# Optimization experiments

Hardware: AMD Instinct MI355X
Metric: run time of the kernel (lower is better)

## Reference

```python
import jax, jax.numpy as jnp
import numpy as np

NUM_EMBEDDINGS = 8192
EMBEDDING_DIM = 256
PROJECTION_DIM = 128


def setup_inputs() -> dict:
    key = jax.random.key(0)
    k_x, k_cb, k_w, k_b = jax.random.split(key, 4)
    x = jax.random.normal(k_x, (16, 1024, EMBEDDING_DIM), dtype=jnp.float32)
    codebook = jax.random.normal(k_cb, (NUM_EMBEDDINGS, EMBEDDING_DIM), dtype=jnp.float32)
    proj_w = jax.random.normal(k_w, (EMBEDDING_DIM, PROJECTION_DIM), dtype=jnp.float32) / np.sqrt(EMBEDDING_DIM)
    proj_b = jax.random.normal(k_b, (PROJECTION_DIM,), dtype=jnp.float32) * 0.01
    return {"x": x, "codebook": codebook, "proj_w": proj_w, "proj_b": proj_b}


def reference(x, codebook, proj_w, proj_b):
    # Flatten tokens: [N, D]
    x_flat = x.reshape(-1, EMBEDDING_DIM)
    # Project tokens and codebook into the distance space: [N, P], [K, P]
    x_proj = x_flat @ proj_w + proj_b
    cb_proj = codebook @ proj_w + proj_b
    # Squared euclidean distances via expansion: [N, K]
    distances = (
        jnp.sum(x_proj ** 2, axis=1, keepdims=True)
        - 2.0 * (x_proj @ cb_proj.T)
        + jnp.sum(cb_proj ** 2, axis=1)
    )
    idx = jnp.argmin(distances, axis=1)
    discrete = jax.nn.one_hot(idx, NUM_EMBEDDINGS, dtype=x.dtype)  # [N, K]
    # One-hot matmul lookup (disguised gather): [N, D]
    quantized = (discrete @ codebook).reshape(x.shape)
    return (discrete, quantized)
```

## Files before the change

### kernel.cpp

```cpp
#include <hip/hip_runtime.h>
#include <math.h>

#define D 256
#define P 128
#define K 8192
#define NTOK 16384
#define NROWS (NTOK + K)
#define CAPC 64
#define MARGIN 3.0f
#define FLT_BIG 3.402823466e+38f

typedef __attribute__((ext_vector_type(8))) short bf16x8;
typedef __attribute__((ext_vector_type(4))) float f32x4;
typedef __attribute__((ext_vector_type(8))) unsigned short u16x8;

__device__ __forceinline__ unsigned short f32_to_bf16_rne(float f) {
    unsigned int u = __float_as_uint(f);
    u = (u + 0x7fffu + ((u >> 16) & 1u)) >> 16;
    return (unsigned short)u;
}

__global__ __launch_bounds__(256) void proj_kernel(
    const float* __restrict__ x, const float* __restrict__ cb,
    const float* __restrict__ w, const float* __restrict__ bias,
    float* __restrict__ xproj, float* __restrict__ cproj,
    float* __restrict__ xnorm, float* __restrict__ cnorm,
    unsigned short* __restrict__ xh, unsigned short* __restrict__ chs,
    int* __restrict__ cnt)
{
    __shared__ float As[16][D];
    const int tid = threadIdx.x;
    const int row0 = blockIdx.x * 16;

    {
        int g = blockIdx.x * 256 + tid;
        if (g < NTOK) cnt[g] = 0;
    }

    for (int i = tid; i < 16 * (D / 4); i += 256) {
        int r = i / (D / 4);
        int c4 = i % (D / 4);
        int gr = row0 + r;
        const float* src = (gr < NTOK) ? (x + (size_t)gr * D)
                                       : (cb + (size_t)(gr - NTOK) * D);
        float4 v = ((const float4*)src)[c4];
        ((float4*)&As[r][0])[c4] = v;
    }
    __syncthreads();

    const int r = tid >> 4;
    const int c0 = (tid & 15) * 8;

    float acc[8];
#pragma unroll
    for (int j = 0; j < 8; j++) acc[j] = 0.f;

    for (int d = 0; d < D; d += 4) {
        float4 a4 = *(const float4*)&As[r][d];
#pragma unroll
        for (int dd = 0; dd < 4; dd++) {
            float av = (dd == 0) ? a4.x : (dd == 1) ? a4.y : (dd == 2) ? a4.z : a4.w;
            float4 w0 = *(const float4*)&w[(size_t)(d + dd) * P + c0];
            float4 w1 = *(const float4*)&w[(size_t)(d + dd) * P + c0 + 4];
            acc[0] = fmaf(av, w0.x, acc[0]);
            acc[1] = fmaf(av, w0.y, acc[1]);
            acc[2] = fmaf(av, w0.z, acc[2]);
            acc[3] = fmaf(av, w0.w, acc[3]);
            acc[4] = fmaf(av, w1.x, acc[4]);
            acc[5] = fmaf(av, w1.y, acc[5]);
            acc[6] = fmaf(av, w1.z, acc[6]);
            acc[7] = fmaf(av, w1.w, acc[7]);
        }
    }

    float out[8];
    float nrm = 0.f;
    u16x8 hv;
#pragma unroll
    for (int j = 0; j < 8; j++) {
        out[j] = acc[j] + bias[c0 + j];
        nrm = fmaf(out[j], out[j], nrm);
        hv[j] = f32_to_bf16_rne(out[j]);
    }

    const int gr = row0 + r;
    float4 o0; o0.x = out[0]; o0.y = out[1]; o0.z = out[2]; o0.w = out[3];
    float4 o1; o1.x = out[4]; o1.y = out[5]; o1.z = out[6]; o1.w = out[7];
    if (gr < NTOK) {
        float* dst = xproj + (size_t)gr * P;
        *(float4*)&dst[c0] = o0;
        *(float4*)&dst[c0 + 4] = o1;
        *(u16x8*)(xh + (size_t)gr * P + c0) = hv;
    } else {
        int row = gr - NTOK;
        float* dst = cproj + (size_t)row * P;
        *(float4*)&dst[c0] = o0;
        *(float4*)&dst[c0 + 4] = o1;
        int t64 = row >> 6, rg = (row >> 4) & 3, rl = row & 15;
        int ks = c0 >> 5, q = (c0 >> 3) & 3;
        size_t atom = ((size_t)(t64 * 16 + rg * 4 + ks) * 4 + q) * 16 + rl;
        *(u16x8*)(chs + atom * 8) = hv;
    }

#pragma unroll
    for (int off = 1; off < 16; off <<= 1)
        nrm += __shfl_xor(nrm, off, 16);
    if ((tid & 15) == 0) {
        if (gr < NTOK) xnorm[gr] = nrm;
        else           cnorm[gr - NTOK] = nrm;
    }
}

__global__ __launch_bounds__(256, 3) void minzero_collect_kernel(
    const unsigned short* __restrict__ xh, const unsigned short* __restrict__ chs,
    const float* __restrict__ xnorm, const float* __restrict__ cnorm,
    int* __restrict__ cnt, int* __restrict__ cand, float* __restrict__ discrete)
{
    const int tid = threadIdx.x;
    const int tok0 = blockIdx.x * 128;
    const int kbase = blockIdx.y * 2048;
    const int flat = blockIdx.y * gridDim.x + blockIdx.x;

    const int wave = tid >> 6;
    const int lane = tid & 63;
    const int quad = lane >> 4;
    const int l15 = lane & 15;
    const int trow = tok0 + wave * 32;

    f32x4* zbase = (f32x4*)discrete + (size_t)flat * 65536;
    const f32x4 zv = (f32x4)(0.f);

    bf16x8 afrag[2][4];
#pragma unroll
    for (int mi = 0; mi < 2; mi++)
#pragma unroll
        for (int ks = 0; ks < 4; ks++)
            afrag[mi][ks] = *(const bf16x8*)(
                xh + (size_t)(trow + mi * 16 + l15) * P + ks * 32 + quad * 8);

    float xnv[2][4];
#pragma unroll
    for (int mi = 0; mi < 2; mi++)
#pragma unroll
        for (int r = 0; r < 4; r++)
            xnv[mi][r] = xnorm[trow + mi * 16 + quad * 4 + r];

    float rmin[2][4];
#pragma unroll
    for (int mi = 0; mi < 2; mi++)
#pragma unroll
        for (int r = 0; r < 4; r++) rmin[mi][r] = FLT_BIG;

    for (int ct = 0; ct < 32; ct++) {
        const int kt = kbase + ct * 64;
        const int t64 = kt >> 6;

#pragma unroll
        for (int s = 0; s < 8; s++)
            zbase[(size_t)ct * 2048 + s * 256 + tid] = zv;

        f32x4 acc[2][4];
#pragma unroll
        for (int mi = 0; mi < 2; mi++)
#pragma unroll
            for (int nj = 0; nj < 4; nj++) acc[mi][nj] = (f32x4)(0.f);

#pragma unroll
        for (int ks = 0; ks < 4; ks++) {
            const bf16x8* base = (const bf16x8*)(chs) + (size_t)(t64 * 16 + ks) * 64 + lane;
            bf16x8 b0 = base[0 * 4 * 64];
            bf16x8 b1 = base[1 * 4 * 64];
            bf16x8 b2 = base[2 * 4 * 64];
            bf16x8 b3 = base[3 * 4 * 64];
            acc[0][0] = __builtin_amdgcn_mfma_f32_16x16x32_bf16(afrag[0][ks], b0, acc[0][0], 0, 0, 0);
            acc[0][1] = __builtin_amdgcn_mfma_f32_16x16x32_bf16(afrag[0][ks], b1, acc[0][1], 0, 0, 0);
            acc[0][2] = __builtin_amdgcn_mfma_f32_16x16x32_bf16(afrag[0][ks], b2, acc[0][2], 0, 0, 0);
            acc[0][3] = __builtin_amdgcn_mfma_f32_16x16x32_bf16(afrag[0][ks], b3, acc[0][3], 0, 0, 0);
            acc[1][0] = __builtin_amdgcn_mfma_f32_16x16x32_bf16(afrag[1][ks], b0, acc[1][0], 0, 0, 0);
            acc[1][1] = __builtin_amdgcn_mfma_f32_16x16x32_bf16(afrag[1][ks], b1, acc[1][1], 0, 0, 0);
            acc[1][2] = __builtin_amdgcn_mfma_f32_16x16x32_bf16(afrag[1][ks], b2, acc[1][2], 0, 0, 0);
            acc[1][3] = __builtin_amdgcn_mfma_f32_16x16x32_bf16(afrag[1][ks], b3, acc[1][3], 0, 0, 0);
        }

        float cn[4];
#pragma unroll
        for (int nj = 0; nj < 4; nj++) cn[nj] = cnorm[kt + nj * 16 + l15];

        if (ct == 0) {
#pragma unroll
            for (int mi = 0; mi < 2; mi++)
#pragma unroll
                for (int r = 0; r < 4; r++) {
                    float rm = rmin[mi][r];
#pragma unroll
                    for (int nj = 0; nj < 4; nj++) {
                        float dd = (xnv[mi][r] - 2.0f * acc[mi][nj][r]) + cn[nj];
                        rm = fminf(rm, dd);
                    }
#pragma unroll
                    for (int off = 1; off < 16; off <<= 1)
                        rm = fminf(rm, __shfl_xor(rm, off));
                    rmin[mi][r] = rm;
                    const float thr = rm + MARGIN;
                    const int tok = trow + mi * 16 + quad * 4 + r;
#pragma unroll
                    for (int nj = 0; nj < 4; nj++) {
                        float dd = (xnv[mi][r] - 2.0f * acc[mi][nj][r]) + cn[nj];
                        if (dd <= thr) {
                            int pos = atomicAdd(&cnt[tok], 1);
                            if (pos < CAPC) cand[(size_t)tok * CAPC + pos] = kt + nj * 16 + l15;
                        }
                    }
                }
        } else {
#pragma unroll
            for (int mi = 0; mi < 2; mi++)
#pragma unroll
                for (int r = 0; r < 4; r++) {
                    float rm = rmin[mi][r];
                    const float thr = rm + MARGIN;
                    const int tok = trow + mi * 16 + quad * 4 + r;
#pragma unroll
                    for (int nj = 0; nj < 4; nj++) {
                        float dd = (xnv[mi][r] - 2.0f * acc[mi][nj][r]) + cn[nj];
                        rm = fminf(rm, dd);
                        if (dd <= thr) {
                            int pos = atomicAdd(&cnt[tok], 1);
                            if (pos < CAPC) cand[(size_t)tok * CAPC + pos] = kt + nj * 16 + l15;
                        }
                    }
                    rmin[mi][r] = rm;
                }
            if (ct & 1) {
#pragma unroll
                for (int mi = 0; mi < 2; mi++)
#pragma unroll
                    for (int r = 0; r < 4; r++) {
                        float m = rmin[mi][r];
#pragma unroll
                        for (int off = 1; off < 16; off <<= 1)
                            m = fminf(m, __shfl_xor(m, off));
                        rmin[mi][r] = m;
                    }
            }
        }
    }
}

__global__ __launch_bounds__(256) void rescorefinal_kernel(
    const float* __restrict__ xproj, const float* __restrict__ cproj,
    const float* __restrict__ xnorm, const float* __restrict__ cnorm,
    const int* __restrict__ cnt, const int* __restrict__ cand,
    const float* __restrict__ cb,
    float* __restrict__ discrete, float* __restrict__ quant)
{
    __shared__ int sidx[64];
    const int tid = threadIdx.x;
    const int lane = tid & 63;
    const int wave = tid >> 6;
    const int tok0 = blockIdx.x * 64;

    for (int i = 0; i < 16; i++) {
        const int t = tok0 + wave * 16 + i;
        const int n = cnt[t];
        const bool full = (n > CAPC);
        const int lim = full ? K : n;
        const float xn = xnorm[t];
        const float* xr = xproj + (size_t)t * P;

        unsigned long long pack = 0xFFFFFFFFFFFFFFFFull;
        for (int j = lane; j < lim; j += 64) {
            const int k = full ? j : cand[(size_t)t * CAPC + j];
            const float* cr = cproj + (size_t)k * P;
            float s = 0.f;
#pragma unroll 8
            for (int p = 0; p < P; p += 4) {
                float4 a = *(const float4*)&xr[p];
                float4 b = *(const float4*)&cr[p];
                s = fmaf(a.x, b.x, s);
                s = fmaf(a.y, b.y, s);
                s = fmaf(a.z, b.z, s);
                s = fmaf(a.w, b.w, s);
            }
            float dist = (xn - 2.0f * s) + cnorm[k];
            unsigned long long pk =
                ((unsigned long long)__float_as_uint(dist) << 32) |
                (unsigned long long)(unsigned)k;
            if (pk < pack) pack = pk;
        }
#pragma unroll
        for (int off = 1; off < 64; off <<= 1) {
            unsigned long long o = __shfl_xor((long long)pack, off);
            if (o < pack) pack = o;
        }
        if (lane == 0) {
            int bi = (int)(pack & 0xFFFFFFFFull);
            if (bi >= 0 && bi < K) {
                sidx[wave * 16 + i] = bi;
                discrete[(size_t)t * K + bi] = 1.0f;
            } else sidx[wave * 16 + i] = 0;
        }
    }
    __syncthreads();

    for (int i = tid; i < 64 * (D / 4); i += 256) {
        int t = i >> 6;
        int c4 = i & 63;
        int bi = sidx[t];
        float4 v = ((const float4*)(cb + (size_t)bi * D))[c4];
        ((float4*)(quant + (size_t)(tok0 + t) * D))[c4] = v;
    }
}

extern "C" void kernel_launch(void* const* d_in, const int* in_sizes, int n_in,
                              void* d_out, int out_size, void* d_ws, size_t ws_size,
                              hipStream_t stream) {
    const float* x    = (const float*)d_in[0];
    const float* cb   = (const float*)d_in[1];
    const float* w    = (const float*)d_in[2];
    const float* bias = (const float*)d_in[3];

    float* out = (float*)d_out;
    float* discrete = out;
    float* quant = out + (size_t)NTOK * K;

    char* ws = (char*)d_ws;
    size_t off = 0;
    float* xproj = (float*)(ws + off); off += (size_t)NTOK * P * 4;
    float* cproj = (float*)(ws + off); off += (size_t)K * P * 4;
    float* xnorm = (float*)(ws + off); off += (size_t)NTOK * 4;
    float* cnorm = (float*)(ws + off); off += (size_t)K * 4;
    unsigned short* xh  = (unsigned short*)(ws + off); off += (size_t)NTOK * P * 2;
    unsigned short* chs = (unsigned short*)(ws + off); off += (size_t)K * P * 2;
    int* cnt  = (int*)(ws + off); off += (size_t)NTOK * 4;
    int* cand = (int*)(ws + off); off += (size_t)NTOK * CAPC * 4;

    proj_kernel<<<dim3(NROWS / 16), dim3(256), 0, stream>>>(
        x, cb, w, bias, xproj, cproj, xnorm, cnorm, xh, chs, cnt);

    minzero_collect_kernel<<<dim3(NTOK / 128, 4), dim3(256), 0, stream>>>(
        xh, chs, xnorm, cnorm, cnt, cand, discrete);

    rescorefinal_kernel<<<dim3(NTOK / 64), dim3(256), 0, stream>>>(
        xproj, cproj, xnorm, cnorm, cnt, cand, cb, discrete, quant);
}
```

Before: 844.2 us.

## Redistribute discrete zero-fill across all three kernels to balance store bandwidth

```diff
diff --git a/kernel.cpp b/kernel.cpp
--- a/kernel.cpp
+++ b/kernel.cpp
@@ -10,6 +10,7 @@
 #define MARGIN 3.0f
 #define FLT_BIG 3.402823466e+38f
 
+
 typedef __attribute__((ext_vector_type(8))) short bf16x8;
 typedef __attribute__((ext_vector_type(4))) float f32x4;
 typedef __attribute__((ext_vector_type(8))) unsigned short u16x8;
@@ -26,7 +27,7 @@
     float* __restrict__ xproj, float* __restrict__ cproj,
     float* __restrict__ xnorm, float* __restrict__ cnorm,
     unsigned short* __restrict__ xh, unsigned short* __restrict__ chs,
-    int* __restrict__ cnt)
+    int* __restrict__ cnt, float* __restrict__ discrete)
 {
     __shared__ float As[16][D];
     const int tid = threadIdx.x;
@@ -55,7 +56,19 @@
 #pragma unroll
     for (int j = 0; j < 8; j++) acc[j] = 0.f;
 
+    const f32x4 zv = (f32x4)(0.f);
+    f32x4* dis4 = (f32x4*)discrete;
+    const int frow0 = 5 * (int)blockIdx.x;
+
     for (int d = 0; d < D; d += 4) {
+        {
+            int j = d >> 2;
+            if (j < 25) {
+                int fr = frow0 + j / 5;
+                int fc4 = 768 + (j % 5) * 256 + tid;
+                dis4[(size_t)fr * 2048 + fc4] = zv;
+            }
+        }
         float4 a4 = *(const float4*)&As[r][d];
 #pragma unroll
         for (int dd = 0; dd < 4; dd++) {
@@ -127,7 +140,8 @@
     const int l15 = lane & 15;
     const int trow = tok0 + wave * 32;
 
-    f32x4* zbase = (f32x4*)discrete + (size_t)flat * 65536;
+    f32x4* dis4 = (f32x4*)discrete;
+    const int frow0 = 7680 + 17 * flat;
     const f32x4 zv = (f32x4)(0.f);
 
     bf16x8 afrag[2][4];
@@ -156,8 +170,14 @@
         const int t64 = kt >> 6;
 
 #pragma unroll
-        for (int s = 0; s < 8; s++)
-            zbase[(size_t)ct * 2048 + s * 256 + tid] = zv;
+        for (int s = 0; s < 3; s++) {
+            int u = ct * 3 + s;
+            if (u < 85) {
+                int fr = frow0 + u / 5;
+                int fc4 = 768 + (u % 5) * 256 + tid;
+                dis4[(size_t)fr * 2048 + fc4] = zv;
+            }
+        }
 
         f32x4 acc[2][4];
 #pragma unroll
@@ -260,7 +280,17 @@
     const int wave = tid >> 6;
     const int tok0 = blockIdx.x * 64;
 
+    f32x4* dis4 = (f32x4*)discrete;
+    const f32x4 zv = (f32x4)(0.f);
+
     for (int i = 0; i < 16; i++) {
+#pragma unroll
+        for (int s = 0; s < 12; s++) {
+            int fr = tok0 + i * 4 + s / 3;
+            int fc4 = (s % 3) * 256 + tid;
+            dis4[(size_t)fr * 2048 + fc4] = zv;
+        }
+
         const int t = tok0 + wave * 16 + i;
         const int n = cnt[t];
         const bool full = (n > CAPC);
@@ -295,18 +325,21 @@
         }
         if (lane == 0) {
             int bi = (int)(pack & 0xFFFFFFFFull);
-            if (bi >= 0 && bi < K) {
-                sidx[wave * 16 + i] = bi;
-                discrete[(size_t)t * K + bi] = 1.0f;
-            } else sidx[wave * 16 + i] = 0;
+            sidx[wave * 16 + i] = (bi >= 0 && bi < K) ? bi : -1;
         }
     }
     __syncthreads();
+
+    if (tid < 64) {
+        int bi = sidx[tid];
+        if (bi >= 0) discrete[(size_t)(tok0 + tid) * K + bi] = 1.0f;
+    }
 
     for (int i = tid; i < 64 * (D / 4); i += 256) {
         int t = i >> 6;
         int c4 = i & 63;
         int bi = sidx[t];
+        if (bi < 0) bi = 0;
         float4 v = ((const float4*)(cb + (size_t)bi * D))[c4];
         ((float4*)(quant + (size_t)(tok0 + t) * D))[c4] = v;
     }
@@ -336,7 +369,7 @@
     int* cand = (int*)(ws + off); off += (size_t)NTOK * CAPC * 4;
 
     proj_kernel<<<dim3(NROWS / 16), dim3(256), 0, stream>>>(
-        x, cb, w, bias, xproj, cproj, xnorm, cnorm, xh, chs, cnt);
+        x, cb, w, bias, xproj, cproj, xnorm, cnorm, xh, chs, cnt, discrete);
 
     minzero_collect_kernel<<<dim3(NTOK / 128, 4), dim3(256), 0, stream>>>(
         xh, chs, xnorm, cnorm, cnt, cand, discrete);
```

New measurement: 872.0 us. 1.03x slower.

## Split one-hot zero-fill of discrete output across all three kernels

Applied to the files above, without the earlier changes.

```diff
diff --git a/kernel.cpp b/kernel.cpp
--- a/kernel.cpp
+++ b/kernel.cpp
@@ -9,6 +9,8 @@
 #define CAPC 64
 #define MARGIN 3.0f
 #define FLT_BIG 3.402823466e+38f
+#define PFILL 256
+
 
 typedef __attribute__((ext_vector_type(8))) short bf16x8;
 typedef __attribute__((ext_vector_type(4))) float f32x4;
@@ -26,14 +28,28 @@
     float* __restrict__ xproj, float* __restrict__ cproj,
     float* __restrict__ xnorm, float* __restrict__ cnorm,
     unsigned short* __restrict__ xh, unsigned short* __restrict__ chs,
-    int* __restrict__ cnt)
+    int* __restrict__ cnt, float* __restrict__ discrete)
 {
     __shared__ float As[16][D];
     const int tid = threadIdx.x;
-    const int row0 = blockIdx.x * 16;
+
+    if (blockIdx.x < PFILL) {
+        const int f = blockIdx.x;
+        f32x4* dis4 = (f32x4*)discrete;
+        const f32x4 zv = (f32x4)(0.f);
+        for (int u = tid; u < 64 * 256; u += 256) {
+            int fr = (f << 6) + (u >> 8);
+            int fc4 = 512 + (u & 255);
+            dis4[(size_t)fr * 2048 + fc4] = zv;
+        }
+        return;
+    }
+
+    const int cblk = blockIdx.x - PFILL;
+    const int row0 = cblk * 16;
 
     {
-        int g = blockIdx.x * 256 + tid;
+        int g = cblk * 256 + tid;
         if (g < NTOK) cnt[g] = 0;
     }
 
@@ -127,7 +143,8 @@
     const int l15 = lane & 15;
     const int trow = tok0 + wave * 32;
 
-    f32x4* zbase = (f32x4*)discrete + (size_t)flat * 65536;
+    f32x4* dis4 = (f32x4*)discrete;
+    const int zrow = flat * 32;
     const f32x4 zv = (f32x4)(0.f);
 
     bf16x8 afrag[2][4];
@@ -154,10 +171,6 @@
     for (int ct = 0; ct < 32; ct++) {
         const int kt = kbase + ct * 64;
         const int t64 = kt >> 6;
-
-#pragma unroll
-        for (int s = 0; s < 8; s++)
-            zbase[(size_t)ct * 2048 + s * 256 + tid] = zv;
 
         f32x4 acc[2][4];
 #pragma unroll
@@ -244,6 +257,13 @@
                     }
             }
         }
+
+        {
+            f32x4* rowp = dis4 + (size_t)(zrow + ct) * 2048;
+#pragma unroll
+            for (int s = 0; s < 5; s++)
+                rowp[768 + s * 256 + tid] = zv;
+        }
     }
 }
 
@@ -259,6 +279,8 @@
     const int lane = tid & 63;
     const int wave = tid >> 6;
     const int tok0 = blockIdx.x * 64;
+
+    float4* dis4f = (float4*)discrete;
 
     for (int i = 0; i < 16; i++) {
         const int t = tok0 + wave * 16 + i;
@@ -293,13 +315,23 @@
             unsigned long long o = __shfl_xor((long long)pack, off);
             if (o < pack) pack = o;
         }
-        if (lane == 0) {
-            int bi = (int)(pack & 0xFFFFFFFFull);
-            if (bi >= 0 && bi < K) {
-                sidx[wave * 16 + i] = bi;
-                discrete[(size_t)t * K + bi] = 1.0f;
-            } else sidx[wave * 16 + i] = 0;
-        }
+        int bi = (int)(pack & 0xFFFFFFFFull);
+        const bool valid = (bi >= 0 && bi < K);
+        if (lane == 0) sidx[wave * 16 + i] = valid ? bi : 0;
+
+#pragma unroll
+        for (int s = 0; s < 8; s++) {
+            int fc4 = s * 64 + lane;
+            int b0 = fc4 << 2;
+            float4 v;
+            v.x = (bi == b0)     ? 1.f : 0.f;
+            v.y = (bi == b0 + 1) ? 1.f : 0.f;
+            v.z = (bi == b0 + 2) ? 1.f : 0.f;
+            v.w = (bi == b0 + 3) ? 1.f : 0.f;
+            dis4f[(size_t)t * 2048 + fc4] = v;
+        }
+        if (lane == 0 && valid && bi >= 2048)
+            discrete[(size_t)t * K + bi] = 1.0f;
     }
     __syncthreads();
 
@@ -335,8 +367,8 @@
     int* cnt  = (int*)(ws + off); off += (size_t)NTOK * 4;
     int* cand = (int*)(ws + off); off += (size_t)NTOK * CAPC * 4;
 
-    proj_kernel<<<dim3(NROWS / 16), dim3(256), 0, stream>>>(
-        x, cb, w, bias, xproj, cproj, xnorm, cnorm, xh, chs, cnt);
+    proj_kernel<<<dim3(NROWS / 16 + PFILL), dim3(256), 0, stream>>>(
+        x, cb, w, bias, xproj, cproj, xnorm, cnorm, xh, chs, cnt, discrete);
 
     minzero_collect_kernel<<<dim3(NTOK / 128, 4), dim3(256), 0, stream>>>(
         xh, chs, xnorm, cnorm, cnt, cand, discrete);
```

After: 850.0 us. Within noise of the previous version (+0.7%).

## Fuse rescore into collect kernel via last-block atomic counter; zero own rows

Applied to the files above, without the earlier changes.

```diff
diff --git a/kernel.cpp b/kernel.cpp
--- a/kernel.cpp
+++ b/kernel.cpp
@@ -26,7 +26,7 @@
     float* __restrict__ xproj, float* __restrict__ cproj,
     float* __restrict__ xnorm, float* __restrict__ cnorm,
     unsigned short* __restrict__ xh, unsigned short* __restrict__ chs,
-    int* __restrict__ cnt)
+    int* __restrict__ cnt, int* __restrict__ done)
 {
     __shared__ float As[16][D];
     const int tid = threadIdx.x;
@@ -35,6 +35,7 @@
     {
         int g = blockIdx.x * 256 + tid;
         if (g < NTOK) cnt[g] = 0;
+        if (g < NTOK / 128) done[g] = 0;
     }
 
     for (int i = tid; i < 16 * (D / 4); i += 256) {
@@ -111,15 +112,17 @@
     }
 }
 
-__global__ __launch_bounds__(256, 3) void minzero_collect_kernel(
+__global__ __launch_bounds__(256, 3) void mzc_rescore_kernel(
     const unsigned short* __restrict__ xh, const unsigned short* __restrict__ chs,
     const float* __restrict__ xnorm, const float* __restrict__ cnorm,
-    int* __restrict__ cnt, int* __restrict__ cand, float* __restrict__ discrete)
+    const float* __restrict__ xproj, const float* __restrict__ cproj,
+    const float* __restrict__ cb,
+    int* __restrict__ cnt, int* __restrict__ cand, int* __restrict__ done,
+    float* __restrict__ discrete, float* __restrict__ quant)
 {
     const int tid = threadIdx.x;
     const int tok0 = blockIdx.x * 128;
     const int kbase = blockIdx.y * 2048;
-    const int flat = blockIdx.y * gridDim.x + blockIdx.x;
 
     const int wave = tid >> 6;
     const int lane = tid & 63;
@@ -127,7 +130,7 @@
     const int l15 = lane & 15;
     const int trow = tok0 + wave * 32;
 
-    f32x4* zbase = (f32x4*)discrete + (size_t)flat * 65536;
+    f32x4* dis4 = (f32x4*)discrete;
     const f32x4 zv = (f32x4)(0.f);
 
     bf16x8 afrag[2][4];
@@ -154,10 +157,6 @@
     for (int ct = 0; ct < 32; ct++) {
         const int kt = kbase + ct * 64;
         const int t64 = kt >> 6;
-
-#pragma unroll
-        for (int s = 0; s < 8; s++)
-            zbase[(size_t)ct * 2048 + s * 256 + tid] = zv;
 
         f32x4 acc[2][4];
 #pragma unroll
@@ -244,24 +243,26 @@
                     }
             }
         }
-    }
-}
-
-__global__ __launch_bounds__(256) void rescorefinal_kernel(
-    const float* __restrict__ xproj, const float* __restrict__ cproj,
-    const float* __restrict__ xnorm, const float* __restrict__ cnorm,
-    const int* __restrict__ cnt, const int* __restrict__ cand,
-    const float* __restrict__ cb,
-    float* __restrict__ discrete, float* __restrict__ quant)
-{
-    __shared__ int sidx[64];
-    const int tid = threadIdx.x;
-    const int lane = tid & 63;
-    const int wave = tid >> 6;
-    const int tok0 = blockIdx.x * 64;
-
-    for (int i = 0; i < 16; i++) {
-        const int t = tok0 + wave * 16 + i;
+
+        {
+            f32x4* rowp = dis4 + (size_t)(tok0 + ct * 4) * 2048 + (size_t)blockIdx.y * 512;
+#pragma unroll
+            for (int s = 0; s < 8; s++)
+                rowp[(size_t)(s >> 1) * 2048 + (s & 1) * 256 + tid] = zv;
+        }
+    }
+
+    __shared__ int s_old;
+    __threadfence();
+    __syncthreads();
+    if (tid == 0) s_old = atomicAdd(&done[blockIdx.x], 1);
+    __syncthreads();
+    if (s_old != 3) return;
+    __threadfence();
+
+    __shared__ int sidx[128];
+    for (int i = 0; i < 32; i++) {
+        const int t = tok0 + wave * 32 + i;
         const int n = cnt[t];
         const bool full = (n > CAPC);
         const int lim = full ? K : n;
@@ -296,16 +297,16 @@
         if (lane == 0) {
             int bi = (int)(pack & 0xFFFFFFFFull);
             if (bi >= 0 && bi < K) {
-                sidx[wave * 16 + i] = bi;
+                sidx[wave * 32 + i] = bi;
                 discrete[(size_t)t * K + bi] = 1.0f;
-            } else sidx[wave * 16 + i] = 0;
+            } else sidx[wave * 32 + i] = 0;
         }
     }
     __syncthreads();
 
-    for (int i = tid; i < 64 * (D / 4); i += 256) {
-        int t = i >> 6;
-        int c4 = i & 63;
+    for (int u = tid; u < 128 * (D / 4); u += 256) {
+        int t = u >> 6;
+        int c4 = u & 63;
         int bi = sidx[t];
         float4 v = ((const float4*)(cb + (size_t)bi * D))[c4];
         ((float4*)(quant + (size_t)(tok0 + t) * D))[c4] = v;
@@ -334,13 +335,11 @@
     unsigned short* chs = (unsigned short*)(ws + off); off += (size_t)K * P * 2;
     int* cnt  = (int*)(ws + off); off += (size_t)NTOK * 4;
     int* cand = (int*)(ws + off); off += (size_t)NTOK * CAPC * 4;
+    int* done = (int*)(ws + off); off += (size_t)(NTOK / 128) * 4;
 
     proj_kernel<<<dim3(NROWS / 16), dim3(256), 0, stream>>>(
-        x, cb, w, bias, xproj, cproj, xnorm, cnorm, xh, chs, cnt);
-
-    minzero_collect_kernel<<<dim3(NTOK / 128, 4), dim3(256), 0, stream>>>(
-        xh, chs, xnorm, cnorm, cnt, cand, discrete);
-
-    rescorefinal_kernel<<<dim3(NTOK / 64), dim3(256), 0, stream>>>(
-        xproj, cproj, xnorm, cnorm, cnt, cand, cb, discrete, quant);
+        x, cb, w, bias, xproj, cproj, xnorm, cnorm, xh, chs, cnt, done);
+
+    mzc_rescore_kernel<<<dim3(NTOK / 128, 4), dim3(256), 0, stream>>>(
+        xh, chs, xnorm, cnorm, xproj, cproj, cb, cnt, cand, done, discrete, quant);
 }
```

Measured after the change: 1.001 ms. 18.6% more time.
